# Optimization experiments

Measured on AMD Instinct MI355X. Metric: run time of the kernel, lower is better.

Reference implementation:

```python
import jax, jax.numpy as jnp
import numpy as np

SEMANTIC_DIM = 128
N_COMPONENTS = 2
EMBED_DIM = SEMANTIC_DIM * N_COMPONENTS  # 256
MAX_LEN = 512


def sinusoidal_pe(max_len, d_model):
    pos = jnp.arange(max_len, dtype=jnp.float32)[:, None]              # (L,1)
    div = jnp.exp(jnp.arange(0, d_model, 2, dtype=jnp.float32) * (-np.log(10000.0) / d_model))
    ang = pos * div                                                     # (L, d/2)
    # interleave sin/cos: pe[:,0::2]=sin, pe[:,1::2]=cos
    return jnp.stack([jnp.sin(ang), jnp.cos(ang)], axis=-1).reshape(max_len, d_model)


def setup_inputs() -> dict:
    key = jax.random.key(0)
    k1, k2, k3, k4 = jax.random.split(key, 4)
    byte_sequence = jax.random.randint(k1, (64, 512), 0, 256, dtype=jnp.int64)
    continuous_positions = jax.random.uniform(k2, (64, 2048), dtype=jnp.float32)
    emb_table = jax.random.normal(k3, (256, EMBED_DIM), dtype=jnp.float32)
    locality_shapes = jax.random.normal(k4, (256, 3), dtype=jnp.float32)
    return {
        "byte_sequence": byte_sequence,
        "continuous_positions": continuous_positions,
        "emb_table": emb_table,
        "locality_shapes": locality_shapes,
    }


def reference(byte_sequence, continuous_positions, emb_table, locality_shapes):
    B, L = byte_sequence.shape
    pe = sinusoidal_pe(MAX_LEN, EMBED_DIM)[:L]                          # (L, E)
    byte_embeds = emb_table[byte_sequence] + pe[None, :, :]             # (B, L, E)
    byte_amplitudes = byte_embeds.reshape(B, L, N_COMPONENTS, SEMANTIC_DIM)

    byte_positions = jnp.linspace(0.0, 1.0, L, dtype=jnp.float32)      # (L,)
    x_diff = continuous_positions[:, :, None] - byte_positions[None, None, :]  # (B, P, L)

    lp = locality_shapes[byte_sequence]                                 # (B, L, 3)
    widths = jnp.abs(lp[:, :, 1]) * 0.02 + 1e-5                         # (B, L)
    amplitudes = jax.nn.sigmoid(lp[:, :, 2])                            # (B, L)

    local_basis = jnp.exp(-0.5 * (x_diff / widths[:, None, :]) ** 2) * amplitudes[:, None, :]
    semantic_field = jnp.einsum('bpl,blcd->bpcd', local_basis, byte_amplitudes)
    return semantic_field
```

## Files before the change

### kernel.cpp

```cpp
#include <hip/hip_runtime.h>
#include <math.h>

#define LSEQ 512
#define EDIM 256
#define PDIM 2048
#define BM   128
#define BK   32
#define NT   16

typedef _Float16 f16x8  __attribute__((ext_vector_type(8)));
typedef _Float16 f16x2  __attribute__((ext_vector_type(2)));
typedef float    f32x16 __attribute__((ext_vector_type(16)));

#if __has_builtin(__builtin_amdgcn_exp2f)
#define EXP2F(x) __builtin_amdgcn_exp2f(x)
#else
#define EXP2F(x) __expf((x) * 0.6931471805599453f)
#endif

__device__ inline f16x2 pk2(float a, float b) {
#if __has_builtin(__builtin_amdgcn_cvt_pkrtz)
    return __builtin_bit_cast(f16x2, __builtin_amdgcn_cvt_pkrtz(a, b));
#else
    f16x2 r; r[0] = (_Float16)a; r[1] = (_Float16)b; return r;
#endif
}

__device__ inline float hw_sin(float ang) {
#if __has_builtin(__builtin_amdgcn_sinf)
    float rev = ang * 0.15915494309189535f;
    float fr  = rev - floorf(rev);
    return __builtin_amdgcn_sinf(fr);
#else
    return sinf(ang);
#endif
}
__device__ inline float hw_cos(float ang) {
#if __has_builtin(__builtin_amdgcn_cosf)
    float rev = ang * 0.15915494309189535f;
    float fr  = rev - floorf(rev);
    return __builtin_amdgcn_cosf(fr);
#else
    return cosf(ang);
#endif
}

__device__ __host__ inline int tile_off(int r, int g) {
    return ((r >> 1) << 6) + ((r & 1) << 5) + (((g ^ ((r >> 1) & 3)) & 3) << 3);
}

__device__ inline void g2lds16(const void* g, void* l) {
    __builtin_amdgcn_global_load_lds(
        (const __attribute__((address_space(1))) void*)g,
        (__attribute__((address_space(3))) void*)l, 16, 0, 0);
}

__global__ __launch_bounds__(256) void precompute_all(
    const int*   __restrict__ bs,
    const float* __restrict__ ls,
    const float* __restrict__ emb,
    float2*      __restrict__ params,
    _Float16*    __restrict__ baset) {
    const int b   = blockIdx.x >> 4;
    const int t   = blockIdx.x & 15;
    const int tid = threadIdx.x;

    __shared__ int sByte[BK];
    if (tid < BK) {
        const int l    = t * BK + tid;
        const int byte = bs[b * LSEQ + l];
        sByte[tid] = byte;
        const float l1  = ls[byte * 3 + 1];
        const float l2  = ls[byte * 3 + 2];
        const float wdt = fabsf(l1) * 0.02f + 1e-5f;
        const float amp = 1.0f / (1.0f + __expf(-l2));
        params[b * LSEQ + l] = make_float2(-0.72134752f / (wdt * wdt),
                                           __log2f(amp));
    }
    __syncthreads();

    const float div = __expf((float)(tid >> 1) * (-2.0f * 9.210340372f / 256.0f));
    _Float16* chunk = baset + ((size_t)blockIdx.x << 13);
#pragma unroll
    for (int g = 0; g < 4; ++g) {
        f16x8 v;
#pragma unroll
        for (int j = 0; j < 8; ++j) {
            const int lj  = g * 8 + j;
            const float ang = (float)(t * BK + lj) * div;
            const float pev = (tid & 1) ? hw_cos(ang) : hw_sin(ang);
            v[j] = (_Float16)(emb[sByte[lj] * EDIM + tid] + pev);
        }
        *(f16x8*)&chunk[tile_off(tid, g)] = v;
    }
}

__global__ __launch_bounds__(512, 4) void field_mfma(
    const float*    __restrict__ cpos,
    const float2*   __restrict__ params,
    const _Float16* __restrict__ baset,
    float*          __restrict__ out) {

    __shared__ __align__(16) _Float16 sW[2][BM * BK];
    __shared__ __align__(16) _Float16 sB[2][EDIM * BK];
    __shared__ __align__(16) float2   sPrm[LSEQ];

    const int orig = blockIdx.x;
    const int wg   = (orig & 7) * 128 + (orig >> 3);
    const int b    = wg >> 4;
    const int pt   = wg & 15;

    const int tid = threadIdx.x, lane = tid & 63, wave = tid >> 6;
    const int l31 = lane & 31, h = lane >> 5;
    const int wrow = wave >> 2, wcol = wave & 3;

    const int sp = tid >> 2;
    const int sg = tid & 3;
    const float mypos = cpos[b * PDIM + pt * BM + sp];
    const float invL  = 1.0f / (float)(LSEQ - 1);
    const int   woff  = tile_off(sp, sg);

    int aoff[2][2], boff[2][2];
#pragma unroll
    for (int rt = 0; rt < 2; ++rt)
#pragma unroll
        for (int kk = 0; kk < 2; ++kk)
            aoff[rt][kk] = tile_off(wrow * 64 + rt * 32 + l31, kk * 2 + h);
#pragma unroll
    for (int ct = 0; ct < 2; ++ct)
#pragma unroll
        for (int kk = 0; kk < 2; ++kk)
            boff[ct][kk] = tile_off(wcol * 64 + ct * 32 + l31, kk * 2 + h);

    sPrm[tid] = params[b * LSEQ + tid];
    const _Float16* bt = baset + ((size_t)b * NT << 13);
#pragma unroll
    for (int buf = 0; buf < 2; ++buf) {
        const _Float16* src = bt + buf * 8192 + wave * 1024 + lane * 8;
        g2lds16(src,       &sB[buf][wave * 1024]);
        g2lds16(src + 512, &sB[buf][wave * 1024 + 512]);
    }
    __syncthreads();

    auto genW = [&](int t, int dbuf) {
        const float4* qp = (const float4*)&sPrm[t * BK + sg * 8];
        const float4 q01 = qp[0], q23 = qp[1], q45 = qp[2], q67 = qp[3];
        const float bl0 = (float)(t * BK + sg * 8) * invL;
        const float pd  = mypos - bl0;
        float w[8];
#define GW(i, c2, la) { float d = pd - (float)(i) * invL; \
                        w[i] = EXP2F(fmaf(d * d, (c2), (la))); }
        GW(0, q01.x, q01.y) GW(1, q01.z, q01.w)
        GW(2, q23.x, q23.y) GW(3, q23.z, q23.w)
        GW(4, q45.x, q45.y) GW(5, q45.z, q45.w)
        GW(6, q67.x, q67.y) GW(7, q67.z, q67.w)
#undef GW
        f16x8 wv;
        ((f16x2*)&wv)[0] = pk2(w[0], w[1]);
        ((f16x2*)&wv)[1] = pk2(w[2], w[3]);
        ((f16x2*)&wv)[2] = pk2(w[4], w[5]);
        ((f16x2*)&wv)[3] = pk2(w[6], w[7]);
        *(f16x8*)&sW[dbuf][woff] = wv;
    };

    genW(0, 0);
    __syncthreads();

    f32x16 acc[2][2];
#pragma unroll
    for (int i = 0; i < 2; ++i)
#pragma unroll
        for (int j = 0; j < 2; ++j) acc[i][j] = (f32x16)(0.f);

    for (int t = 0; t < NT; ++t) {
        const int cur = t & 1;
        if (t < NT - 1) genW(t + 1, cur ^ 1);

        const _Float16* wb = sW[cur];
        const _Float16* bb = sB[cur];
        __builtin_amdgcn_s_setprio(1);
#pragma unroll
        for (int kk = 0; kk < 2; ++kk) {
            f16x8 fa[2], fb[2];
#pragma unroll
            for (int rt = 0; rt < 2; ++rt) fa[rt] = *(const f16x8*)&wb[aoff[rt][kk]];
#pragma unroll
            for (int ct = 0; ct < 2; ++ct) fb[ct] = *(const f16x8*)&bb[boff[ct][kk]];
#pragma unroll
            for (int ct = 0; ct < 2; ++ct)
#pragma unroll
                for (int rt = 0; rt < 2; ++rt)
                    acc[rt][ct] = __builtin_amdgcn_mfma_f32_32x32x16_f16(fa[rt], fb[ct], acc[rt][ct], 0, 0, 0);
        }
        __builtin_amdgcn_s_setprio(0);

        __syncthreads();

        if (t < NT - 2) {
            const _Float16* src = bt + (t + 2) * 8192 + wave * 1024 + lane * 8;
            g2lds16(src,       &sB[cur][wave * 1024]);
            g2lds16(src + 512, &sB[cur][wave * 1024 + 512]);
        }
    }

#pragma unroll
    for (int rt = 0; rt < 2; ++rt)
#pragma unroll
        for (int ct = 0; ct < 2; ++ct) {
            const int e = wcol * 64 + ct * 32 + l31;
            const int pbase = pt * BM + wrow * 64 + rt * 32 + 4 * h;
#pragma unroll
            for (int reg = 0; reg < 16; ++reg) {
                const int p = pbase + (reg & 3) + 8 * (reg >> 2);
                out[((size_t)b * PDIM + p) * EDIM + e] = acc[rt][ct][reg];
            }
        }
}

extern "C" void kernel_launch(void* const* d_in, const int* in_sizes, int n_in,
                              void* d_out, int out_size, void* d_ws, size_t ws_size,
                              hipStream_t stream) {
    const int*   bs   = (const int*)d_in[0];
    const float* cpos = (const float*)d_in[1];
    const float* emb  = (const float*)d_in[2];
    const float* ls   = (const float*)d_in[3];

    const int B = in_sizes[0] / LSEQ;

    char* ws = (char*)d_ws;
    float2*   params = (float2*)ws;
    _Float16* baset  = (_Float16*)(ws + (1u << 18));

    precompute_all<<<B * NT, 256, 0, stream>>>(bs, ls, emb, params, baset);
    field_mfma<<<B * (PDIM / BM), 512, 0, stream>>>(cpos, params, baset, (float*)d_out);
}
```

Measured before the change: 66.56 us.

## Halve block to four waves, each computing a 64x128 output tile

The field kernel now runs 256 threads instead of 512. Each wave owns a 64x128 slice with eight 32x32 MFMA accumulators instead of four, which raises fragment reuse per LDS read. Each thread generates two weight rows, and the weight parameters are read from global memory into registers instead of being staged through shared memory. The next tile's weight generation is moved after the MFMA block, so it overlaps differently with matrix work. The cost is higher register pressure (128 accumulator registers), fewer waves per block to hide latency, and a lower launch-bounds occupancy hint.

```diff
diff --git a/kernel.cpp b/kernel.cpp
--- a/kernel.cpp
+++ b/kernel.cpp
@@ -29,8 +29,7 @@
 __device__ inline float hw_sin(float ang) {
 #if __has_builtin(__builtin_amdgcn_sinf)
     float rev = ang * 0.15915494309189535f;
-    float fr  = rev - floorf(rev);
-    return __builtin_amdgcn_sinf(fr);
+    return __builtin_amdgcn_sinf(rev - floorf(rev));
 #else
     return sinf(ang);
 #endif
@@ -38,8 +37,7 @@
 __device__ inline float hw_cos(float ang) {
 #if __has_builtin(__builtin_amdgcn_cosf)
     float rev = ang * 0.15915494309189535f;
-    float fr  = rev - floorf(rev);
-    return __builtin_amdgcn_cosf(fr);
+    return __builtin_amdgcn_cosf(rev - floorf(rev));
 #else
     return cosf(ang);
 #endif
@@ -95,7 +93,7 @@
     }
 }
 
-__global__ __launch_bounds__(512, 4) void field_mfma(
+__global__ __launch_bounds__(256, 3) void field_mfma(
     const float*    __restrict__ cpos,
     const float2*   __restrict__ params,
     const _Float16* __restrict__ baset,
@@ -103,7 +101,6 @@
 
     __shared__ __align__(16) _Float16 sW[2][BM * BK];
     __shared__ __align__(16) _Float16 sB[2][EDIM * BK];
-    __shared__ __align__(16) float2   sPrm[LSEQ];
 
     const int orig = blockIdx.x;
     const int wg   = (orig & 7) * 128 + (orig >> 3);
@@ -112,102 +109,117 @@
 
     const int tid = threadIdx.x, lane = tid & 63, wave = tid >> 6;
     const int l31 = lane & 31, h = lane >> 5;
-    const int wrow = wave >> 2, wcol = wave & 3;
-
-    const int sp = tid >> 2;
-    const int sg = tid & 3;
-    const float mypos = cpos[b * PDIM + pt * BM + sp];
-    const float invL  = 1.0f / (float)(LSEQ - 1);
-    const int   woff  = tile_off(sp, sg);
-
-    int aoff[2][2], boff[2][2];
-#pragma unroll
-    for (int rt = 0; rt < 2; ++rt)
-#pragma unroll
-        for (int kk = 0; kk < 2; ++kk)
-            aoff[rt][kk] = tile_off(wrow * 64 + rt * 32 + l31, kk * 2 + h);
-#pragma unroll
-    for (int ct = 0; ct < 2; ++ct)
-#pragma unroll
-        for (int kk = 0; kk < 2; ++kk)
-            boff[ct][kk] = tile_off(wcol * 64 + ct * 32 + l31, kk * 2 + h);
-
-    sPrm[tid] = params[b * LSEQ + tid];
+    const int wrow = wave >> 1, wcol = wave & 1;
+
+    const int kg = tid & 3;
+    const int r0 = tid >> 2;
+    const float pos0 = cpos[b * PDIM + pt * BM + r0];
+    const float pos1 = cpos[b * PDIM + pt * BM + r0 + 64];
+    const float invL = 1.0f / (float)(LSEQ - 1);
+    const int woff0 = tile_off(r0, kg);
+    const int woff1 = woff0 + 2048;
+
+    int aoff[2], boff[2];
+#pragma unroll
+    for (int kk = 0; kk < 2; ++kk) {
+        aoff[kk] = tile_off(wrow * 64 + l31, kk * 2 + h);
+        boff[kk] = tile_off(wcol * 128 + l31, kk * 2 + h);
+    }
+
+    const float2* prm = params + b * LSEQ;
     const _Float16* bt = baset + ((size_t)b * NT << 13);
+
 #pragma unroll
     for (int buf = 0; buf < 2; ++buf) {
-        const _Float16* src = bt + buf * 8192 + wave * 1024 + lane * 8;
-        g2lds16(src,       &sB[buf][wave * 1024]);
-        g2lds16(src + 512, &sB[buf][wave * 1024 + 512]);
-    }
-    __syncthreads();
+        const _Float16* src = bt + buf * 8192 + wave * 2048 + lane * 8;
+#pragma unroll
+        for (int i = 0; i < 4; ++i)
+            g2lds16(src + i * 512, &sB[buf][wave * 2048 + i * 512 + lane * 8]);
+    }
+
+    float4 q0, q1, q2, q3;
+    {
+        const float4* qp = (const float4*)(prm + kg * 8);
+        q0 = qp[0]; q1 = qp[1]; q2 = qp[2]; q3 = qp[3];
+    }
 
     auto genW = [&](int t, int dbuf) {
-        const float4* qp = (const float4*)&sPrm[t * BK + sg * 8];
-        const float4 q01 = qp[0], q23 = qp[1], q45 = qp[2], q67 = qp[3];
-        const float bl0 = (float)(t * BK + sg * 8) * invL;
-        const float pd  = mypos - bl0;
-        float w[8];
-#define GW(i, c2, la) { float d = pd - (float)(i) * invL; \
-                        w[i] = EXP2F(fmaf(d * d, (c2), (la))); }
-        GW(0, q01.x, q01.y) GW(1, q01.z, q01.w)
-        GW(2, q23.x, q23.y) GW(3, q23.z, q23.w)
-        GW(4, q45.x, q45.y) GW(5, q45.z, q45.w)
-        GW(6, q67.x, q67.y) GW(7, q67.z, q67.w)
+        const float bl0 = (float)(t * BK + kg * 8) * invL;
+        const float pd0 = pos0 - bl0;
+        const float pd1 = pos1 - bl0;
+        float wa[8], wb[8];
+#define GW(i, c2, la) { float d0 = pd0 - (float)(i) * invL;            \
+                        wa[i] = EXP2F(fmaf(d0 * d0, (c2), (la)));      \
+                        float d1 = pd1 - (float)(i) * invL;            \
+                        wb[i] = EXP2F(fmaf(d1 * d1, (c2), (la))); }
+        GW(0, q0.x, q0.y) GW(1, q0.z, q0.w)
+        GW(2, q1.x, q1.y) GW(3, q1.z, q1.w)
+        GW(4, q2.x, q2.y) GW(5, q2.z, q2.w)
+        GW(6, q3.x, q3.y) GW(7, q3.z, q3.w)
 #undef GW
-        f16x8 wv;
-        ((f16x2*)&wv)[0] = pk2(w[0], w[1]);
-        ((f16x2*)&wv)[1] = pk2(w[2], w[3]);
-        ((f16x2*)&wv)[2] = pk2(w[4], w[5]);
-        ((f16x2*)&wv)[3] = pk2(w[6], w[7]);
-        *(f16x8*)&sW[dbuf][woff] = wv;
+        f16x8 va, vb;
+        ((f16x2*)&va)[0] = pk2(wa[0], wa[1]); ((f16x2*)&va)[1] = pk2(wa[2], wa[3]);
+        ((f16x2*)&va)[2] = pk2(wa[4], wa[5]); ((f16x2*)&va)[3] = pk2(wa[6], wa[7]);
+        ((f16x2*)&vb)[0] = pk2(wb[0], wb[1]); ((f16x2*)&vb)[1] = pk2(wb[2], wb[3]);
+        ((f16x2*)&vb)[2] = pk2(wb[4], wb[5]); ((f16x2*)&vb)[3] = pk2(wb[6], wb[7]);
+        *(f16x8*)&sW[dbuf][woff0] = va;
+        *(f16x8*)&sW[dbuf][woff1] = vb;
     };
 
     genW(0, 0);
     __syncthreads();
 
-    f32x16 acc[2][2];
+    f32x16 acc[2][4];
 #pragma unroll
     for (int i = 0; i < 2; ++i)
 #pragma unroll
-        for (int j = 0; j < 2; ++j) acc[i][j] = (f32x16)(0.f);
+        for (int j = 0; j < 4; ++j) acc[i][j] = (f32x16)(0.f);
 
     for (int t = 0; t < NT; ++t) {
         const int cur = t & 1;
-        if (t < NT - 1) genW(t + 1, cur ^ 1);
-
-        const _Float16* wb = sW[cur];
-        const _Float16* bb = sB[cur];
+
+        if (t < NT - 1) {
+            const float4* qp = (const float4*)(prm + (t + 1) * BK + kg * 8);
+            q0 = qp[0]; q1 = qp[1]; q2 = qp[2]; q3 = qp[3];
+        }
+
+        const _Float16* wb_ = sW[cur];
+        const _Float16* bb_ = sB[cur];
         __builtin_amdgcn_s_setprio(1);
 #pragma unroll
         for (int kk = 0; kk < 2; ++kk) {
-            f16x8 fa[2], fb[2];
-#pragma unroll
-            for (int rt = 0; rt < 2; ++rt) fa[rt] = *(const f16x8*)&wb[aoff[rt][kk]];
-#pragma unroll
-            for (int ct = 0; ct < 2; ++ct) fb[ct] = *(const f16x8*)&bb[boff[ct][kk]];
-#pragma unroll
-            for (int ct = 0; ct < 2; ++ct)
+            f16x8 fa[2], fb[4];
+#pragma unroll
+            for (int rt = 0; rt < 2; ++rt)
+                fa[rt] = *(const f16x8*)&wb_[aoff[kk] + rt * 1024];
+#pragma unroll
+            for (int ct = 0; ct < 4; ++ct)
+                fb[ct] = *(const f16x8*)&bb_[boff[kk] + ct * 1024];
+#pragma unroll
+            for (int ct = 0; ct < 4; ++ct)
 #pragma unroll
                 for (int rt = 0; rt < 2; ++rt)
                     acc[rt][ct] = __builtin_amdgcn_mfma_f32_32x32x16_f16(fa[rt], fb[ct], acc[rt][ct], 0, 0, 0);
         }
         __builtin_amdgcn_s_setprio(0);
 
+        if (t < NT - 1) genW(t + 1, cur ^ 1);
+
         __syncthreads();
 
         if (t < NT - 2) {
-            const _Float16* src = bt + (t + 2) * 8192 + wave * 1024 + lane * 8;
-            g2lds16(src,       &sB[cur][wave * 1024]);
-            g2lds16(src + 512, &sB[cur][wave * 1024 + 512]);
+            const _Float16* src = bt + (t + 2) * 8192 + wave * 2048 + lane * 8;
+#pragma unroll
+            for (int i = 0; i < 4; ++i)
+                g2lds16(src + i * 512, &sB[cur][wave * 2048 + i * 512 + lane * 8]);
         }
     }
 
 #pragma unroll
     for (int rt = 0; rt < 2; ++rt)
 #pragma unroll
-        for (int ct = 0; ct < 2; ++ct) {
-            const int e = wcol * 64 + ct * 32 + l31;
+        for (int ct = 0; ct < 4; ++ct) {
+            const int e = wcol * 128 + ct * 32 + l31;
             const int pbase = pt * BM + wrow * 64 + rt * 32 + 4 * h;
 #pragma unroll
             for (int reg = 0; reg < 16; ++reg) {
@@ -232,5 +244,5 @@
     _Float16* baset  = (_Float16*)(ws + (1u << 18));
 
     precompute_all<<<B * NT, 256, 0, stream>>>(bs, ls, emb, params, baset);
-    field_mfma<<<B * (PDIM / BM), 512, 0, stream>>>(cpos, params, baset, (float*)d_out);
-}
+    field_mfma<<<B * (PDIM / BM), 256, 0, stream>>>(cpos, params, baset, (float*)d_out);
+}
```

New measurement: 81.55 us. 22.5% more time.
